# Optimization experiments

Measured on AMD Instinct MI355X. Metric: run time of the kernel, lower is better.

The kernel has to match this reference:

```python
import jax, jax.numpy as jnp
import numpy as np

# irreps layout: list of (multiplicity, l); same for input and output (square Linear)
IRREPS = [(256, 0), (128, 1), (64, 2)]  # dims: 256 + 384 + 320 = 960
N_NODES = 100000
N_TRIVIAL = 256  # dim of leading 0e block in irreps_out


def setup_inputs() -> dict:
    key = jax.random.key(0)
    ks = jax.random.split(key, 5)
    data_in = jax.random.normal(ks[0], (N_NODES, sum(m * (2 * l + 1) for m, l in IRREPS)), dtype=jnp.float32)
    # weight init matching linear_layer_init: uniform(-a, a), a = sqrt(6/(mul1*mul2 + mul_out)),
    # here mul1 = mul_out = mul, mul2 = 1 -> a = sqrt(6 / (2*mul)) = sqrt(3/mul)
    Ws = {}
    for i, (mul, l) in enumerate(IRREPS):
        a = float(np.sqrt(3.0 / mul))
        Ws[f"W{i}"] = jax.random.uniform(ks[i + 1], (mul, mul), minval=-a, maxval=a, dtype=jnp.float32)
    b = jnp.zeros((N_TRIVIAL,), dtype=jnp.float32)
    return {"data_in": data_in, "W0": Ws["W0"], "W1": Ws["W1"], "W2": Ws["W2"], "b": b}


def reference(data_in, W0, W1, W2, b):
    # FullyConnectedTensorProduct(irreps_in, '1x0e', irreps_out) with x2 = ones reduces to
    # per-irrep block matmul: out_block = (x_block @ W) / sqrt(mul_in)
    # (w3j(l,0,l) = I/sqrt(2l+1) cancels with component-norm sqrt((2l+1)/mul_in)).
    Ws = [W0, W1, W2]
    outs = []
    off = 0
    for (mul, l), W in zip(IRREPS, Ws):
        d = 2 * l + 1
        x = data_in[:, off : off + mul * d].reshape(-1, mul, d)  # [N, mul, 2l+1]
        y = jnp.einsum("bud,uw->bwd", x, W) * (1.0 / np.sqrt(mul))
        outs.append(y.reshape(-1, mul * d))
        off += mul * d
    out = jnp.concatenate(outs, axis=1)
    # bias added only to the leading trivial (0e) block
    out = out.at[:, :N_TRIVIAL].add(b)
    return out
```

## Files before the change

kernel.cpp:

```cpp
#include <hip/hip_runtime.h>

typedef __attribute__((ext_vector_type(8))) short short8;
typedef __attribute__((ext_vector_type(4))) float f32x4;

__device__ __forceinline__ unsigned pack2bf(float x0, float x1) {
    unsigned u0 = __float_as_uint(x0) + 0x8000u;
    unsigned u1 = __float_as_uint(x1) + 0x8000u;
    return __builtin_amdgcn_perm(u1, u0, 0x07060302u);
}

__device__ __forceinline__ void prep_one(const float* __restrict__ W,
                                         unsigned short* __restrict__ dst,
                                         int mul, int shift, float scale, int idx) {
    if (idx >= mul * mul) return;
    int u = idx >> shift;
    int w = idx - (u << shift);
    int nkb = mul >> 5;
    int cb = w >> 4, kb = u >> 5;
    int lane = ((u >> 3) & 3) * 16 + (w & 15);
    int j = u & 7;
    unsigned uv = __float_as_uint(W[idx] * scale) + 0x8000u;
    dst[(((cb * nkb + kb) * 64 + lane) << 3) + j] = (unsigned short)(uv >> 16);
}

__global__ __launch_bounds__(256) void prep_all(const float* __restrict__ W0,
                                                const float* __restrict__ W1,
                                                const float* __restrict__ W2,
                                                unsigned short* __restrict__ wf) {
    int b = blockIdx.x;
    if (b < 256)      prep_one(W0, wf,         256, 8, 0.0625f,              b * 256 + threadIdx.x);
    else if (b < 320) prep_one(W1, wf + 65536, 128, 7, 0.08838834764831845f, (b - 256) * 256 + threadIdx.x);
    else              prep_one(W2, wf + 81920, 64,  6, 0.125f,               (b - 320) * 256 + threadIdx.x);
}

template <int D>
__device__ __forceinline__ void pack_from_lds(const float* __restrict__ lrow, int xr, int c0,
                                              short8* __restrict__ out) {
    float buf[8 * D];
#pragma unroll
    for (int v = 0; v < 2 * D; ++v) {
        f32x4 t = *reinterpret_cast<const f32x4*>(lrow + (((c0 + v) ^ xr) << 2));
        buf[v * 4 + 0] = t[0]; buf[v * 4 + 1] = t[1];
        buf[v * 4 + 2] = t[2]; buf[v * 4 + 3] = t[3];
    }
#pragma unroll
    for (int d = 0; d < D; ++d) {
        union { short8 s8; unsigned u[4]; } fr;
#pragma unroll
        for (int jj = 0; jj < 4; ++jj)
            fr.u[jj] = pack2bf(buf[(2 * jj) * D + d], buf[(2 * jj + 1) * D + d]);
        out[d] = fr.s8;
    }
}

#define ST1(p, val, imm) \
    asm volatile("global_store_dword %0, %1, off offset:" imm :: "v"(p), "v"(val) : "memory")

__global__ __launch_bounds__(256, 1) void lin_main(const float* __restrict__ in,
                                                   const unsigned short* __restrict__ wf0,
                                                   const unsigned short* __restrict__ wf1,
                                                   const unsigned short* __restrict__ wf2,
                                                   const float* __restrict__ bias,
                                                   float* __restrict__ out) {
    __shared__ float lds[2][15360];
    const int w = threadIdx.x >> 6;
    const int lane = threadIdx.x & 63;
    const int lm = lane & 15, lg = lane >> 4, xr = lm & 7;

    short8 b0[4][8], b1[2][4], b2[2];
#pragma unroll
    for (int c = 0; c < 4; ++c)
#pragma unroll
        for (int kb = 0; kb < 8; ++kb)
            b0[c][kb] = *reinterpret_cast<const short8*>(wf0 + ((((w * 4 + c) * 8 + kb) * 64 + lane) << 3));
#pragma unroll
    for (int c = 0; c < 2; ++c)
#pragma unroll
        for (int kb = 0; kb < 4; ++kb)
            b1[c][kb] = *reinterpret_cast<const short8*>(wf1 + ((((w * 2 + c) * 4 + kb) * 64 + lane) << 3));
#pragma unroll
    for (int kb = 0; kb < 2; ++kb)
        b2[kb] = *reinterpret_cast<const short8*>(wf2 + (((w * 2 + kb) * 64 + lane) << 3));
    float bv[4];
#pragma unroll
    for (int c = 0; c < 4; ++c) bv[c] = bias[(w * 4 + c) * 16 + lm];

    int srcoff[15];
#pragma unroll
    for (int i = 0; i < 15; ++i) {
        int s = w * 960 + i * 64 + lane;
        int row = (int)(((long long)s * 17477) >> 22);
        int c = s - row * 240;
        srcoff[i] = (row * 240 + (c ^ (row & 7))) << 4;
    }

    const int b = blockIdx.x;
    const int nt = (b < 106) ? 25 : 24;
    const int t0 = b * 24 + (b < 106 ? b : 106);

#define STAGE5(kk, bufi, ph)                                                              \
    {                                                                                     \
        const char* tb = (const char*)in + (size_t)(t0 + (kk)) * 61440;                   \
        char* sd = (char*)&lds[0][0] + (bufi) * 61440 + w * 15360;                        \
        _Pragma("unroll")                                                                 \
        for (int i = 5 * (ph); i < 5 * (ph) + 5; ++i)                                     \
            __builtin_amdgcn_global_load_lds(                                             \
                (const __attribute__((address_space(1))) void*)(tb + srcoff[i]),          \
                (__attribute__((address_space(3))) void*)(sd + i * 1024), 16, 0, 0);      \
    }

    STAGE5(0, 0, 0);
    STAGE5(0, 0, 1);
    STAGE5(0, 0, 2);
    asm volatile("s_waitcnt vmcnt(0)" ::: "memory");
    __builtin_amdgcn_s_barrier();
    __builtin_amdgcn_sched_barrier(0);

    for (int k = 0; k < nt; ++k) {
        const int par = k & 1;
        const float* lrow = &lds[0][0] + par * 15360 + lm * 960;
        const int trow = (t0 + k) * 16;

        if (k + 1 < nt) STAGE5(k + 1, par ^ 1, 0);
        __builtin_amdgcn_sched_barrier(0);
        short8 a0[8];
#pragma unroll
        for (int kb = 0; kb < 8; ++kb)
            pack_from_lds<1>(lrow, xr, 8 * kb + 2 * lg, &a0[kb]);
        f32x4 acc0[4];
#pragma unroll
        for (int c = 0; c < 4; ++c) {
            f32x4 z = {0.f, 0.f, 0.f, 0.f};
#pragma unroll
            for (int kb = 0; kb < 8; ++kb)
                z = __builtin_amdgcn_mfma_f32_16x16x32_bf16(a0[kb], b0[c][kb], z, 0, 0, 0);
            acc0[c] = z;
        }
        __builtin_amdgcn_sched_barrier(0);

        if (k + 1 < nt) STAGE5(k + 1, par ^ 1, 1);
        __builtin_amdgcn_sched_barrier(0);
        short8 a1[4][3];
#pragma unroll
        for (int kb = 0; kb < 4; ++kb)
            pack_from_lds<3>(lrow, xr, 64 + 24 * kb + 6 * lg, a1[kb]);
        f32x4 acc1[2][3];
#pragma unroll
        for (int c = 0; c < 2; ++c)
#pragma unroll
            for (int d = 0; d < 3; ++d) {
                f32x4 z = {0.f, 0.f, 0.f, 0.f};
#pragma unroll
                for (int kb = 0; kb < 4; ++kb)
                    z = __builtin_amdgcn_mfma_f32_16x16x32_bf16(a1[kb][d], b1[c][kb], z, 0, 0, 0);
                acc1[c][d] = z;
            }
        __builtin_amdgcn_sched_barrier(0);

        if (k + 1 < nt) STAGE5(k + 1, par ^ 1, 2);
        __builtin_amdgcn_sched_barrier(0);
        short8 a2[2][5];
#pragma unroll
        for (int kb = 0; kb < 2; ++kb)
            pack_from_lds<5>(lrow, xr, 160 + 40 * kb + 10 * lg, a2[kb]);
        f32x4 acc2[5];
#pragma unroll
        for (int d = 0; d < 5; ++d) {
            f32x4 z = {0.f, 0.f, 0.f, 0.f};
#pragma unroll
            for (int kb = 0; kb < 2; ++kb)
                z = __builtin_amdgcn_mfma_f32_16x16x32_bf16(a2[kb][d], b2[kb], z, 0, 0, 0);
            acc2[d] = z;
        }

#pragma unroll
        for (int jj = 0; jj < 4; ++jj) {
            float* r = out + (size_t)(trow + lg * 4 + jj) * 960;
            float* p0 = r + w * 64 + lm;
            ST1(p0, acc0[0][jj] + bv[0], "0");
            ST1(p0, acc0[1][jj] + bv[1], "64");
            ST1(p0, acc0[2][jj] + bv[2], "128");
            ST1(p0, acc0[3][jj] + bv[3], "192");
            float* p1 = r + 256 + (w * 32 + lm) * 3;
            ST1(p1, acc1[0][0][jj], "0");
            ST1(p1, acc1[0][1][jj], "4");
            ST1(p1, acc1[0][2][jj], "8");
            ST1(p1, acc1[1][0][jj], "192");
            ST1(p1, acc1[1][1][jj], "196");
            ST1(p1, acc1[1][2][jj], "200");
            float* p2 = r + 640 + (w * 16 + lm) * 5;
            ST1(p2, acc2[0][jj], "0");
            ST1(p2, acc2[1][jj], "4");
            ST1(p2, acc2[2][jj], "8");
            ST1(p2, acc2[3][jj], "12");
            ST1(p2, acc2[4][jj], "16");
        }

        __builtin_amdgcn_sched_barrier(0);
        if (k + 1 < nt)
            asm volatile("s_waitcnt vmcnt(60)" ::: "memory");
        __builtin_amdgcn_s_barrier();
        __builtin_amdgcn_sched_barrier(0);
    }
#undef STAGE5
}

extern "C" void kernel_launch(void* const* d_in, const int* in_sizes, int n_in,
                              void* d_out, int out_size, void* d_ws, size_t ws_size,
                              hipStream_t stream) {
    (void)in_sizes; (void)n_in; (void)out_size; (void)ws_size;
    const float* x  = (const float*)d_in[0];
    const float* W0 = (const float*)d_in[1];
    const float* W1 = (const float*)d_in[2];
    const float* W2 = (const float*)d_in[3];
    const float* b  = (const float*)d_in[4];
    float* out = (float*)d_out;
    unsigned short* wf = (unsigned short*)d_ws;

    prep_all<<<336, 256, 0, stream>>>(W0, W1, W2, wf);
    lin_main<<<256, 256, 0, stream>>>(x, wf, wf + 65536, wf + 81920, b, out);
}
```

Measured before the change: 173.1 us.

## Use triple-buffered LDS staging with direct register loads for last l=2 chunk

Switches the LDS input staging from double to triple buffering, prefetching two tiles ahead. Each row now stages only its first 832 floats through LDS, while the final 160 floats of the l=2 block are loaded straight into registers with global_load_dwordx4 and packed there. This keeps three buffers within the LDS budget and deepens the load pipeline to hide global memory latency. The cost is extra vector registers for the direct loads, more complex vmcnt accounting, and uncoalesced per-lane 160-byte loads.

```diff
diff --git a/kernel.cpp b/kernel.cpp
--- a/kernel.cpp
+++ b/kernel.cpp
@@ -34,6 +34,18 @@
 }
 
 template <int D>
+__device__ __forceinline__ void pack_core(const float* __restrict__ buf, short8* __restrict__ out) {
+#pragma unroll
+    for (int d = 0; d < D; ++d) {
+        union { short8 s8; unsigned u[4]; } fr;
+#pragma unroll
+        for (int jj = 0; jj < 4; ++jj)
+            fr.u[jj] = pack2bf(buf[(2 * jj) * D + d], buf[(2 * jj + 1) * D + d]);
+        out[d] = fr.s8;
+    }
+}
+
+template <int D>
 __device__ __forceinline__ void pack_from_lds(const float* __restrict__ lrow, int xr, int c0,
                                               short8* __restrict__ out) {
     float buf[8 * D];
@@ -43,18 +55,13 @@
         buf[v * 4 + 0] = t[0]; buf[v * 4 + 1] = t[1];
         buf[v * 4 + 2] = t[2]; buf[v * 4 + 3] = t[3];
     }
-#pragma unroll
-    for (int d = 0; d < D; ++d) {
-        union { short8 s8; unsigned u[4]; } fr;
-#pragma unroll
-        for (int jj = 0; jj < 4; ++jj)
-            fr.u[jj] = pack2bf(buf[(2 * jj) * D + d], buf[(2 * jj + 1) * D + d]);
-        out[d] = fr.s8;
-    }
+    pack_core<D>(buf, out);
 }
 
 #define ST1(p, val, imm) \
     asm volatile("global_store_dword %0, %1, off offset:" imm :: "v"(p), "v"(val) : "memory")
+#define DLD(idx, imm) \
+    asm volatile("global_load_dwordx4 %0, %1, off offset:" imm : "=v"(dreg[idx]) : "v"(dptr))
 
 __global__ __launch_bounds__(256, 1) void lin_main(const float* __restrict__ in,
                                                    const unsigned short* __restrict__ wf0,
@@ -62,7 +69,7 @@
                                                    const unsigned short* __restrict__ wf2,
                                                    const float* __restrict__ bias,
                                                    float* __restrict__ out) {
-    __shared__ float lds[2][15360];
+    __shared__ float lds[39936];
     const int w = threadIdx.x >> 6;
     const int lane = threadIdx.x & 63;
     const int lm = lane & 15, lg = lane >> 4, xr = lm & 7;
@@ -85,44 +92,54 @@
 #pragma unroll
     for (int c = 0; c < 4; ++c) bv[c] = bias[(w * 4 + c) * 16 + lm];
 
-    int srcoff[15];
-#pragma unroll
-    for (int i = 0; i < 15; ++i) {
-        int s = w * 960 + i * 64 + lane;
-        int row = (int)(((long long)s * 17477) >> 22);
-        int c = s - row * 240;
-        srcoff[i] = (row * 240 + (c ^ (row & 7))) << 4;
+    int srcoff[13];
+#pragma unroll
+    for (int i = 0; i < 13; ++i) {
+        int q = i * 64 + lane;
+        int r = 0;
+        if (q >= 416) { q -= 416; r = 2; }
+        if (q >= 208) { q -= 208; r += 1; }
+        int row = w * 4 + r;
+        srcoff[i] = row * 3840 + ((q ^ (row & 7)) << 4);
     }
 
     const int b = blockIdx.x;
     const int nt = (b < 106) ? 25 : 24;
     const int t0 = b * 24 + (b < 106 ? b : 106);
 
-#define STAGE5(kk, bufi, ph)                                                              \
+#define STAGE(kk, bi)                                                                     \
     {                                                                                     \
         const char* tb = (const char*)in + (size_t)(t0 + (kk)) * 61440;                   \
-        char* sd = (char*)&lds[0][0] + (bufi) * 61440 + w * 15360;                        \
+        char* sd = (char*)lds + (bi) * 53248 + w * 13312;                                 \
         _Pragma("unroll")                                                                 \
-        for (int i = 5 * (ph); i < 5 * (ph) + 5; ++i)                                     \
+        for (int i = 0; i < 13; ++i)                                                      \
             __builtin_amdgcn_global_load_lds(                                             \
                 (const __attribute__((address_space(1))) void*)(tb + srcoff[i]),          \
                 (__attribute__((address_space(3))) void*)(sd + i * 1024), 16, 0, 0);      \
     }
 
-    STAGE5(0, 0, 0);
-    STAGE5(0, 0, 1);
-    STAGE5(0, 0, 2);
-    asm volatile("s_waitcnt vmcnt(0)" ::: "memory");
+    STAGE(0, 0);
+    STAGE(1, 1);
+    asm volatile("s_waitcnt vmcnt(13)" ::: "memory");
     __builtin_amdgcn_s_barrier();
     __builtin_amdgcn_sched_barrier(0);
 
+    int par3 = 0;
     for (int k = 0; k < nt; ++k) {
-        const int par = k & 1;
-        const float* lrow = &lds[0][0] + par * 15360 + lm * 960;
         const int trow = (t0 + k) * 16;
-
-        if (k + 1 < nt) STAGE5(k + 1, par ^ 1, 0);
-        __builtin_amdgcn_sched_barrier(0);
+        const float* lrow = lds + par3 * 13312 + lm * 832;
+
+        f32x4 dreg[10];
+        const float* dptr = in + (size_t)(t0 + k) * 15360 + lm * 960 + 800 + lg * 40;
+        DLD(0, "0");  DLD(1, "16");  DLD(2, "32");  DLD(3, "48");  DLD(4, "64");
+        DLD(5, "80"); DLD(6, "96");  DLD(7, "112"); DLD(8, "128"); DLD(9, "144");
+        __builtin_amdgcn_sched_barrier(0);
+        if (k + 2 < nt) {
+            int sdst = par3 + 2; if (sdst >= 3) sdst -= 3;
+            STAGE(k + 2, sdst);
+        }
+        __builtin_amdgcn_sched_barrier(0);
+
         short8 a0[8];
 #pragma unroll
         for (int kb = 0; kb < 8; ++kb)
@@ -136,10 +153,6 @@
                 z = __builtin_amdgcn_mfma_f32_16x16x32_bf16(a0[kb], b0[c][kb], z, 0, 0, 0);
             acc0[c] = z;
         }
-        __builtin_amdgcn_sched_barrier(0);
-
-        if (k + 1 < nt) STAGE5(k + 1, par ^ 1, 1);
-        __builtin_amdgcn_sched_barrier(0);
         short8 a1[4][3];
 #pragma unroll
         for (int kb = 0; kb < 4; ++kb)
@@ -155,14 +168,27 @@
                     z = __builtin_amdgcn_mfma_f32_16x16x32_bf16(a1[kb][d], b1[c][kb], z, 0, 0, 0);
                 acc1[c][d] = z;
             }
-        __builtin_amdgcn_sched_barrier(0);
-
-        if (k + 1 < nt) STAGE5(k + 1, par ^ 1, 2);
-        __builtin_amdgcn_sched_barrier(0);
+
+        __builtin_amdgcn_sched_barrier(0);
+        if (k + 2 < nt)
+            asm volatile("s_waitcnt vmcnt(13)" ::: "memory");
+        else
+            asm volatile("s_waitcnt vmcnt(0)" ::: "memory");
+        __builtin_amdgcn_sched_barrier(0);
+
         short8 a2[2][5];
-#pragma unroll
-        for (int kb = 0; kb < 2; ++kb)
-            pack_from_lds<5>(lrow, xr, 160 + 40 * kb + 10 * lg, a2[kb]);
+        pack_from_lds<5>(lrow, xr, 160 + 10 * lg, a2[0]);
+        {
+            float dbuf[40];
+#pragma unroll
+            for (int i = 0; i < 10; ++i) {
+                dbuf[i * 4 + 0] = dreg[i][0];
+                dbuf[i * 4 + 1] = dreg[i][1];
+                dbuf[i * 4 + 2] = dreg[i][2];
+                dbuf[i * 4 + 3] = dreg[i][3];
+            }
+            pack_core<5>(dbuf, a2[1]);
+        }
         f32x4 acc2[5];
 #pragma unroll
         for (int d = 0; d < 5; ++d) {
@@ -197,12 +223,12 @@
         }
 
         __builtin_amdgcn_sched_barrier(0);
-        if (k + 1 < nt)
-            asm volatile("s_waitcnt vmcnt(60)" ::: "memory");
         __builtin_amdgcn_s_barrier();
         __builtin_amdgcn_sched_barrier(0);
-    }
-#undef STAGE5
+
+        par3 += 1; if (par3 == 3) par3 = 0;
+    }
+#undef STAGE
 }
 
 extern "C" void kernel_launch(void* const* d_in, const int* in_sizes, int n_in,
```

After: 182.6 us. 1.05x slower.
